# Optimization experiments

Measured on AMD Instinct MI355X. Metric: run time of the kernel, lower is better.

## Reference

```python
import jax, jax.numpy as jnp
import numpy as np

B, S, HID = 2, 2048, 1024
H, HKV, D = 16, 8, 128
G = H // HKV  # GQA group size
EPS = 1e-6
THETA = 1000000.0


def setup_inputs() -> dict:
    key = jax.random.key(0)
    ks = jax.random.split(key, 6)
    hidden_states = jax.random.normal(ks[0], (B, S, HID), dtype=jnp.float32)
    # causal boolean mask: True = attend
    attention_mask = jnp.tril(jnp.ones((S, S), dtype=bool))[None, None]
    # RoPE tables (HF convention: freqs duplicated across both halves)
    inv_freq = 1.0 / (THETA ** (jnp.arange(0, D, 2, dtype=jnp.float32) / D))
    ang = jnp.arange(S, dtype=jnp.float32)[:, None] * inv_freq[None, :]  # [S, D/2]
    emb = jnp.concatenate([ang, ang], axis=-1)  # [S, D]
    cos, sin = jnp.cos(emb), jnp.sin(emb)
    std = 0.02
    Wq = jax.random.normal(ks[1], (HID, H * D), dtype=jnp.float32) * std
    Wk = jax.random.normal(ks[2], (HID, HKV * D), dtype=jnp.float32) * std
    Wv = jax.random.normal(ks[3], (HID, HKV * D), dtype=jnp.float32) * std
    Wo = jax.random.normal(ks[4], (H * D, HID), dtype=jnp.float32) * std
    q_norm_w = jnp.ones((D,), dtype=jnp.float32)
    k_norm_w = jnp.ones((D,), dtype=jnp.float32)
    return {"hidden_states": hidden_states, "attention_mask": attention_mask,
            "cos": cos, "sin": sin, "Wq": Wq, "Wk": Wk, "Wv": Wv, "Wo": Wo,
            "q_norm_w": q_norm_w, "k_norm_w": k_norm_w}


def _rms_norm(x, w):
    var = jnp.mean(x * x, axis=-1, keepdims=True)
    return x * jax.lax.rsqrt(var + EPS) * w


def _rotate_half(x):
    x1, x2 = jnp.split(x, 2, axis=-1)
    return jnp.concatenate([-x2, x1], axis=-1)


def reference(hidden_states, attention_mask, cos, sin, Wq, Wk, Wv, Wo, q_norm_w, k_norm_w):
    b, s, _ = hidden_states.shape
    xq = (hidden_states @ Wq).reshape(b, s, H, D).transpose(0, 2, 1, 3)    # [B,H,S,D]
    xk = (hidden_states @ Wk).reshape(b, s, HKV, D).transpose(0, 2, 1, 3)  # [B,Hkv,S,D]
    xv = (hidden_states @ Wv).reshape(b, s, HKV, D).transpose(0, 2, 1, 3)  # [B,Hkv,S,D]
    xq = _rms_norm(xq, q_norm_w)
    xk = _rms_norm(xk, k_norm_w)
    c = cos[None, None]  # [1,1,S,D]
    si = sin[None, None]
    xq = xq * c + _rotate_half(xq) * si
    xk = xk * c + _rotate_half(xk) * si
    # GQA without materializing repeated KV: group q heads per kv head
    xqg = xq.reshape(b, HKV, G, s, D)
    scale = 1.0 / jnp.sqrt(jnp.asarray(D, dtype=xq.dtype))
    scores = jnp.einsum('bkgsd,bktd->bkgst', xqg, xk) * scale  # [B,Hkv,G,S,S]
    mask = attention_mask[:, :, None]  # [1,1,1,S,S]
    scores = jnp.where(mask, scores, jnp.asarray(-jnp.inf, dtype=scores.dtype))
    probs = jax.nn.softmax(scores, axis=-1)
    out = jnp.einsum('bkgst,bktd->bkgsd', probs, xv)  # [B,Hkv,G,S,D]
    out = out.reshape(b, H, s, D).transpose(0, 2, 1, 3).reshape(b, s, H * D)
    return out @ Wo
```

## Files before the change

### kernel.cpp

```cpp
#include <hip/hip_runtime.h>
#include <stdint.h>

#define B_ 2
#define S_ 2048
#define H_ 16
#define HKV_ 8
#define D_ 128
#define EPS_ 1e-6f
#define SCALE_ 0.08838834764831845f
#define QSZ_ 8388608
#define KSZ_ 4194304

typedef __attribute__((ext_vector_type(8))) __bf16 bf16x8;
typedef __attribute__((ext_vector_type(4))) float f32x4;
typedef __attribute__((ext_vector_type(16))) float f32x16;

static __device__ __forceinline__ uint16_t f2b(float f) {
  uint32_t u = __builtin_bit_cast(uint32_t, f);
  u += 0x7fffu + ((u >> 16) & 1u);
  return (uint16_t)(u >> 16);
}
static __device__ __forceinline__ float b2f(uint16_t b) {
  uint32_t u = ((uint32_t)b) << 16;
  return __builtin_bit_cast(float, u);
}

typedef const __attribute__((address_space(1))) uint32_t* gas_p;
typedef __attribute__((address_space(3))) uint32_t* las_p;
static __device__ __forceinline__ void gload16(const void* g, void* l) {
  __builtin_amdgcn_global_load_lds((gas_p)g, (las_p)l, 16, 0, 0);
}

__global__ void castk(const float* __restrict__ in, uint16_t* __restrict__ out) {
  int i = blockIdx.x * 256 + threadIdx.x;
  float4 f = ((const float4*)in)[i];
  uint2 o;
  o.x = (uint32_t)f2b(f.x) | ((uint32_t)f2b(f.y) << 16);
  o.y = (uint32_t)f2b(f.z) | ((uint32_t)f2b(f.w) << 16);
  ((uint2*)out)[i] = o;
}

__global__ void transcast(const float* __restrict__ Wm, uint16_t* __restrict__ Wt,
                          int K, int N) {
  __shared__ float t[32][33];
  int nb = blockIdx.x * 32, kb = blockIdx.y * 32;
  int tx = threadIdx.x & 31, ty = threadIdx.x >> 5;
  #pragma unroll
  for (int i = ty; i < 32; i += 8) t[i][tx] = Wm[(size_t)(kb + i) * N + nb + tx];
  __syncthreads();
  #pragma unroll
  for (int i = ty; i < 32; i += 8) Wt[(size_t)(nb + i) * K + kb + tx] = f2b(t[tx][i]);
}

__global__ __launch_bounds__(256) void vtrans(const uint16_t* __restrict__ Vin,
                                              uint16_t* __restrict__ Vt) {
  __shared__ uint16_t L[64 * 64];
  int s0 = blockIdx.x * 64, d0 = blockIdx.y * 64;
  const uint16_t* src = Vin + (size_t)blockIdx.z * S_ * D_;
  uint16_t* dst = Vt + (size_t)blockIdx.z * S_ * D_;
  int t = threadIdx.x;
  int rr = t >> 3, cb = t & 7;
  #pragma unroll
  for (int half = 0; half < 2; ++half) {
    int row = rr + half * 32;
    uint4 v = *(const uint4*)(src + (size_t)(s0 + row) * D_ + d0 + cb * 8);
    *(uint4*)(L + row * 64 + ((cb ^ (row & 7)) * 8)) = v;
  }
  __syncthreads();
  int dr = t >> 2, sc = (t & 3) * 16;
  union { uint16_t s[16]; uint4 q[2]; } u;
  #pragma unroll
  for (int j = 0; j < 16; ++j) {
    int s = sc + j;
    u.s[j] = L[s * 64 + (((dr >> 3) ^ (s & 7)) * 8) + (dr & 7)];
  }
  uint4* op = (uint4*)(dst + (size_t)(d0 + dr) * S_ + s0 + sc);
  op[0] = u.q[0];
  op[1] = u.q[1];
}

__global__ __launch_bounds__(256) void gemm_bt(const uint16_t* __restrict__ A,
                                               const uint16_t* __restrict__ Bt,
                                               void* __restrict__ Cout,
                                               int M, int N, int K, int mode) {
  __shared__ uint16_t Al[128 * 64];
  __shared__ uint16_t Bl[128 * 64];
  int tid = threadIdx.x;
  int lane = tid & 63, lr = lane & 15, g = lane >> 4;
  int w = tid >> 6, wm = w >> 1, wn = w & 1;
  int wbase = w * 64;
  int m0 = blockIdx.y * 128, n0 = blockIdx.x * 128;
  f32x4 acc[4][4] = {};
  for (int k0 = 0; k0 < K; k0 += 64) {
    __syncthreads();
    #pragma unroll
    for (int p = 0; p < 4; ++p) {
      int c = tid + p * 256;
      int row = c >> 3, cb = c & 7;
      int sc = (cb ^ (row & 7)) * 8;
      gload16(A + (size_t)(m0 + row) * K + k0 + sc, Al + (size_t)(p * 256 + wbase) * 8);
      gload16(Bt + (size_t)(n0 + row) * K + k0 + sc, Bl + (size_t)(p * 256 + wbase) * 8);
    }
    __syncthreads();
    #pragma unroll
    for (int ks = 0; ks < 2; ++ks) {
      bf16x8 af[4], bfr[4];
      #pragma unroll
      for (int mi = 0; mi < 4; ++mi) {
        int row = wm * 64 + mi * 16 + lr;
        af[mi] = *(bf16x8*)((char*)Al + row * 128 + ((ks * 64 + g * 16) ^ ((row & 7) << 4)));
      }
      #pragma unroll
      for (int ni = 0; ni < 4; ++ni) {
        int row = wn * 64 + ni * 16 + lr;
        bfr[ni] = *(bf16x8*)((char*)Bl + row * 128 + ((ks * 64 + g * 16) ^ ((row & 7) << 4)));
      }
      __builtin_amdgcn_s_setprio(1);
      #pragma unroll
      for (int mi = 0; mi < 4; ++mi)
        #pragma unroll
        for (int ni = 0; ni < 4; ++ni)
          acc[mi][ni] = __builtin_amdgcn_mfma_f32_16x16x32_bf16(af[mi], bfr[ni], acc[mi][ni], 0, 0, 0);
      __builtin_amdgcn_s_setprio(0);
    }
  }
  #pragma unroll
  for (int mi = 0; mi < 4; ++mi)
    #pragma unroll
    for (int ni = 0; ni < 4; ++ni)
      #pragma unroll
      for (int e = 0; e < 4; ++e) {
        int row = m0 + wm * 64 + mi * 16 + 4 * g + e;
        int col = n0 + wn * 64 + ni * 16 + lr;
        float v = acc[mi][ni][e];
        if (mode == 2) {
          ((float*)Cout)[(size_t)row * N + col] = v;
        } else {
          int bb = row >> 11, s = row & 2047;
          size_t off;
          if (col < 2048)
            off = (((size_t)(bb * 16 + (col >> 7))) * 2048 + s) * 128 + (col & 127);
          else if (col < 3072)
            off = QSZ_ + (((size_t)(bb * 8 + ((col - 2048) >> 7))) * 2048 + s) * 128 + (col & 127);
          else
            off = QSZ_ + KSZ_ + (((size_t)(bb * 8 + ((col - 3072) >> 7))) * 2048 + s) * 128 + (col & 127);
          ((uint16_t*)Cout)[off] = f2b(v);
        }
      }
}

__global__ void norm_rope(uint16_t* __restrict__ Qb, uint16_t* __restrict__ Kb,
                          const float* __restrict__ qw, const float* __restrict__ kw,
                          const float* __restrict__ cosr, const float* __restrict__ sinr) {
  int row = blockIdx.x * 4 + (threadIdx.x >> 6);
  int lane = threadIdx.x & 63;
  int hh = row % 24;
  int bs = row / 24;
  int b = bs >> 11, s = bs & 2047;
  uint16_t* ptr;
  const float* wv;
  float sc;
  if (hh < H_) { ptr = Qb + (((size_t)(b * H_ + hh)) * S_ + s) * D_; wv = qw; sc = SCALE_; }
  else         { ptr = Kb + (((size_t)(b * HKV_ + (hh - H_))) * S_ + s) * D_; wv = kw; sc = 1.0f; }
  float x1 = b2f(ptr[lane]), x2 = b2f(ptr[lane + 64]);
  float ss = x1 * x1 + x2 * x2;
  #pragma unroll
  for (int msk = 1; msk < 64; msk <<= 1) ss += __shfl_xor(ss, msk, 64);
  float r = rsqrtf(ss * (1.0f / 128.0f) + EPS_);
  float n1 = x1 * r * wv[lane], n2 = x2 * r * wv[lane + 64];
  float c1 = cosr[s * 128 + lane], s1 = sinr[s * 128 + lane];
  float c2 = cosr[s * 128 + lane + 64], s2 = sinr[s * 128 + lane + 64];
  ptr[lane]      = f2b((n1 * c1 - n2 * s1) * sc);
  ptr[lane + 64] = f2b((n2 * c2 + n1 * s2) * sc);
}

#define STAGE(BUF, KB) {                                                       \
  int kb64 = (KB) * 64;                                                        \
  _Pragma("unroll") for (int p2 = 0; p2 < 4; ++p2) {                           \
    int ck = p2 * 4 + w;                                                       \
    int krow = ck * 4 + (lane >> 4);                                           \
    int kg = (lane & 15) ^ (krow & 7);                                         \
    gload16(Kg + (size_t)(kb64 + krow) * D_ + kg * 8, Kl[BUF] + ck * 512);     \
    int vrow = ck * 8 + (lane >> 3);                                           \
    int vg = (lane & 7) ^ (vrow & 7);                                          \
    gload16(Vg + (size_t)vrow * S_ + kb64 + vg * 8, Vl[BUF] + ck * 512);       \
  } }

__global__ __launch_bounds__(256, 2) void attn_kernel(const uint16_t* __restrict__ Qb,
                                                      const uint16_t* __restrict__ Kb,
                                                      const uint16_t* __restrict__ Vtg,
                                                      uint16_t* __restrict__ out) {
  __shared__ uint16_t Kl[2][64 * 128];
  __shared__ uint16_t Vl[2][128 * 64];
  int tid = threadIdx.x, lane = tid & 63, w = tid >> 6;
  int ql = lane & 31, hi = lane >> 5;
  int bi = blockIdx.x;
  int qg = 15 - (bi >> 5);
  int rem = bi & 31;
  int bkv = rem >> 1, hsel = rem & 1;
  int b = bkv >> 3, kv = bkv & 7, h = kv * 2 + hsel;
  int qt = qg * 4 + w;
  int q0 = qt * 32;
  int mykb = qt >> 1;
  int kbmax = 2 * qg + 1;
  const uint16_t* Qg = Qb + ((size_t)(b * H_ + h)) * S_ * D_;
  const uint16_t* Kg = Kb + ((size_t)(b * HKV_ + kv)) * S_ * D_;
  const uint16_t* Vg = Vtg + ((size_t)(b * HKV_ + kv)) * S_ * D_;
  bf16x8 qf[8];
  #pragma unroll
  for (int t = 0; t < 8; ++t)
    qf[t] = *(const bf16x8*)(Qg + (size_t)(q0 + ql) * D_ + t * 16 + 8 * hi);
  f32x16 O[4] = {};
  float mrun = -__builtin_inff();
  float lrun = 0.f;
  STAGE(0, 0)
  for (int kb = 0; kb <= kbmax; ++kb) {
    int cur = kb & 1;
    __syncthreads();
    if (kb < kbmax) STAGE(cur ^ 1, kb + 1)
    if (kb <= mykb) {
      const uint16_t* KlC = Kl[cur];
      const uint16_t* VlC = Vl[cur];
      bool diag = (kb == mykb);
      bool skip2 = diag && ((qt & 1) == 0);
      float p0[16], p1[16];
      {
        bf16x8 kf[8];
        #pragma unroll
        for (int t = 0; t < 8; ++t)
          kf[t] = *(const bf16x8*)(KlC + ql * 128 + (((2 * t + hi) ^ (ql & 7)) * 8));
        f32x16 acc = {};
        __builtin_amdgcn_s_setprio(1);
        #pragma unroll
        for (int t = 0; t < 8; ++t)
          acc = __builtin_amdgcn_mfma_f32_32x32x16_bf16(kf[t], qf[t], acc, 0, 0, 0);
        __builtin_amdgcn_s_setprio(0);
        #pragma unroll
        for (int r = 0; r < 16; ++r) p0[r] = acc[r];
      }
      if (!skip2) {
        bf16x8 kf[8];
        #pragma unroll
        for (int t = 0; t < 8; ++t)
          kf[t] = *(const bf16x8*)(KlC + (32 + ql) * 128 + (((2 * t + hi) ^ (ql & 7)) * 8));
        f32x16 acc = {};
        __builtin_amdgcn_s_setprio(1);
        #pragma unroll
        for (int t = 0; t < 8; ++t)
          acc = __builtin_amdgcn_mfma_f32_32x32x16_bf16(kf[t], qf[t], acc, 0, 0, 0);
        __builtin_amdgcn_s_setprio(0);
        #pragma unroll
        for (int r = 0; r < 16; ++r) p1[r] = acc[r];
      }
      if (diag && !(qt & 1)) {
        #pragma unroll
        for (int r = 0; r < 16; ++r) {
          int kk = kb * 64 + 8 * (r >> 2) + 4 * hi + (r & 3);
          if (kk > q0 + ql) p0[r] = -__builtin_inff();
        }
      }
      if (diag && (qt & 1)) {
        #pragma unroll
        for (int r = 0; r < 16; ++r) {
          int kk = kb * 64 + 32 + 8 * (r >> 2) + 4 * hi + (r & 3);
          if (kk > q0 + ql) p1[r] = -__builtin_inff();
        }
      }
      float m8[8];
      #pragma unroll
      for (int i = 0; i < 8; ++i) m8[i] = fmaxf(p0[i], p0[i + 8]);
      if (!skip2) {
        #pragma unroll
        for (int i = 0; i < 8; ++i) m8[i] = fmaxf(m8[i], fmaxf(p1[i], p1[i + 8]));
      }
      float m4a = fmaxf(m8[0], m8[4]), m4b = fmaxf(m8[1], m8[5]);
      float m4c = fmaxf(m8[2], m8[6]), m4d = fmaxf(m8[3], m8[7]);
      float pmax = fmaxf(fmaxf(m4a, m4b), fmaxf(m4c, m4d));
      pmax = fmaxf(pmax, __shfl_xor(pmax, 32, 64));
      if (__any(pmax > mrun + 8.f)) {
        float mnew = fmaxf(mrun, pmax);
        float rs = __expf(mrun - mnew);
        lrun *= rs;
        #pragma unroll
        for (int r = 0; r < 16; ++r) {
          float rr = __shfl(rs, (r & 3) + 8 * (r >> 2) + 4 * hi, 64);
          #pragma unroll
          for (int dt = 0; dt < 4; ++dt) O[dt][r] *= rr;
        }
        mrun = mnew;
      }
      float ls = 0.f;
      union PW { uint32_t w[4]; bf16x8 v; } pa0, pa1;
      #pragma unroll
      for (int r = 0; r < 16; ++r) { p0[r] = __expf(p0[r] - mrun); ls += p0[r]; }
      {
        uint32_t uu[4][2];
        #pragma unroll
        for (int T = 0; T < 4; ++T) {
          asm("v_cvt_pk_bf16_f32 %0, %1, %2" : "=v"(uu[T][0]) : "v"(p0[4 * T]), "v"(p0[4 * T + 1]));
          asm("v_cvt_pk_bf16_f32 %0, %1, %2" : "=v"(uu[T][1]) : "v"(p0[4 * T + 2]), "v"(p0[4 * T + 3]));
        }
        uint32_t a = uu[0][0], bb2 = uu[1][0];
        asm("v_permlane32_swap_b32 %0, %1" : "+v"(a), "+v"(bb2));
        uint32_t c = uu[0][1], d = uu[1][1];
        asm("v_permlane32_swap_b32 %0, %1" : "+v"(c), "+v"(d));
        pa0.w[0] = a; pa0.w[1] = c; pa0.w[2] = bb2; pa0.w[3] = d;
        uint32_t a2 = uu[2][0], b2 = uu[3][0];
        asm("v_permlane32_swap_b32 %0, %1" : "+v"(a2), "+v"(b2));
        uint32_t c2 = uu[2][1], d2 = uu[3][1];
        asm("v_permlane32_swap_b32 %0, %1" : "+v"(c2), "+v"(d2));
        pa1.w[0] = a2; pa1.w[1] = c2; pa1.w[2] = b2; pa1.w[3] = d2;
      }
      __builtin_amdgcn_s_setprio(1);
      #pragma unroll
      for (int dt = 0; dt < 4; ++dt) {
        bf16x8 v0 = *(const bf16x8*)(VlC + (dt * 32 + ql) * 64 + (((0 + hi) ^ (ql & 7)) * 8));
        bf16x8 v1 = *(const bf16x8*)(VlC + (dt * 32 + ql) * 64 + (((2 + hi) ^ (ql & 7)) * 8));
        O[dt] = __builtin_amdgcn_mfma_f32_32x32x16_bf16(pa0.v, v0, O[dt], 0, 0, 0);
        O[dt] = __builtin_amdgcn_mfma_f32_32x32x16_bf16(pa1.v, v1, O[dt], 0, 0, 0);
      }
      __builtin_amdgcn_s_setprio(0);
      if (!skip2) {
        union PW pa2, pa3;
        #pragma unroll
        for (int r = 0; r < 16; ++r) { p1[r] = __expf(p1[r] - mrun); ls += p1[r]; }
        {
          uint32_t uu[4][2];
          #pragma unroll
          for (int T = 0; T < 4; ++T) {
            asm("v_cvt_pk_bf16_f32 %0, %1, %2" : "=v"(uu[T][0]) : "v"(p1[4 * T]), "v"(p1[4 * T + 1]));
            asm("v_cvt_pk_bf16_f32 %0, %1, %2" : "=v"(uu[T][1]) : "v"(p1[4 * T + 2]), "v"(p1[4 * T + 3]));
          }
          uint32_t a = uu[0][0], bb2 = uu[1][0];
          asm("v_permlane32_swap_b32 %0, %1" : "+v"(a), "+v"(bb2));
          uint32_t c = uu[0][1], d = uu[1][1];
          asm("v_permlane32_swap_b32 %0, %1" : "+v"(c), "+v"(d));
          pa2.w[0] = a; pa2.w[1] = c; pa2.w[2] = bb2; pa2.w[3] = d;
          uint32_t a2 = uu[2][0], b2 = uu[3][0];
          asm("v_permlane32_swap_b32 %0, %1" : "+v"(a2), "+v"(b2));
          uint32_t c2 = uu[2][1], d2 = uu[3][1];
          asm("v_permlane32_swap_b32 %0, %1" : "+v"(c2), "+v"(d2));
          pa3.w[0] = a2; pa3.w[1] = c2; pa3.w[2] = b2; pa3.w[3] = d2;
        }
        __builtin_amdgcn_s_setprio(1);
        #pragma unroll
        for (int dt = 0; dt < 4; ++dt) {
          bf16x8 v2 = *(const bf16x8*)(VlC + (dt * 32 + ql) * 64 + (((4 + hi) ^ (ql & 7)) * 8));
          bf16x8 v3 = *(const bf16x8*)(VlC + (dt * 32 + ql) * 64 + (((6 + hi) ^ (ql & 7)) * 8));
          O[dt] = __builtin_amdgcn_mfma_f32_32x32x16_bf16(pa2.v, v2, O[dt], 0, 0, 0);
          O[dt] = __builtin_amdgcn_mfma_f32_32x32x16_bf16(pa3.v, v3, O[dt], 0, 0, 0);
        }
        __builtin_amdgcn_s_setprio(0);
      }
      ls += __shfl_xor(ls, 32, 64);
      lrun += ls;
    }
  }
  float linv = 1.0f / lrun;
  #pragma unroll
  for (int r = 0; r < 16; ++r) {
    int qrl = (r & 3) + 8 * (r >> 2) + 4 * hi;
    float lr_ = __shfl(linv, qrl, 64);
    #pragma unroll
    for (int dt = 0; dt < 4; ++dt) {
      size_t o = ((size_t)(b * S_ + q0 + qrl)) * 2048 + h * 128 + dt * 32 + ql;
      out[o] = f2b(O[dt][r] * lr_);
    }
  }
}

extern "C" void kernel_launch(void* const* d_in, const int* in_sizes, int n_in,
                              void* d_out, int out_size, void* d_ws, size_t ws_size,
                              hipStream_t stream) {
  const float* hidden = (const float*)d_in[0];
  const float* cosr = (const float*)d_in[2];
  const float* sinr = (const float*)d_in[3];
  const float* Wq = (const float*)d_in[4];
  const float* Wk = (const float*)d_in[5];
  const float* Wv = (const float*)d_in[6];
  const float* Wo = (const float*)d_in[7];
  const float* qw = (const float*)d_in[8];
  const float* kw = (const float*)d_in[9];

  uint16_t* p = (uint16_t*)d_ws;
  uint16_t* Xb   = p; p += (size_t)4096 * 1024;
  uint16_t* Wqt  = p; p += (size_t)2048 * 1024;
  uint16_t* Wkt  = p; p += (size_t)1024 * 1024;
  uint16_t* Wvt  = p; p += (size_t)1024 * 1024;
  uint16_t* Wot  = p; p += (size_t)1024 * 2048;
  uint16_t* Qbuf = p; p += (size_t)B_ * H_ * S_ * D_;
  uint16_t* Kbuf = p; p += (size_t)B_ * HKV_ * S_ * D_;
  uint16_t* Vbuf = p; p += (size_t)B_ * HKV_ * S_ * D_;
  uint16_t* attn = p; p += (size_t)4096 * 2048;
  uint16_t* Vtb  = Xb;

  castk<<<4096, 256, 0, stream>>>(hidden, Xb);
  transcast<<<dim3(64, 32), 256, 0, stream>>>(Wq, Wqt, 1024, 2048);
  transcast<<<dim3(32, 32), 256, 0, stream>>>(Wk, Wkt, 1024, 1024);
  transcast<<<dim3(32, 32), 256, 0, stream>>>(Wv, Wvt, 1024, 1024);
  transcast<<<dim3(32, 64), 256, 0, stream>>>(Wo, Wot, 2048, 1024);
  gemm_bt<<<dim3(32, 32), 256, 0, stream>>>(Xb, Wqt, Qbuf, 4096, 4096, 1024, 3);
  vtrans<<<dim3(32, 2, 16), 256, 0, stream>>>(Vbuf, Vtb);
  norm_rope<<<24576, 256, 0, stream>>>(Qbuf, Kbuf, qw, kw, cosr, sinr);
  attn_kernel<<<512, 256, 0, stream>>>(Qbuf, Kbuf, Vtb, attn);
  gemm_bt<<<dim3(8, 32), 256, 0, stream>>>(attn, Wot, d_out, 4096, 1024, 2048, 2);
}
```

Before: 204.6 us.

## Add smaller-tile output GEMM and interleave causal attention block order

Adds a dedicated output-projection GEMM with 128x64 tiles, which launches 512 blocks instead of 256 so more of the GPU's compute units stay busy for the final fp32 projection. The attention grid mapping now sends the first 256 blocks to the heaviest query groups first and the second 256 to the lightest first. This is meant to balance causal work across the two waves of blocks. Smaller tiles reduce reuse per block and add redundant A loads.

```diff
diff --git a/kernel.cpp b/kernel.cpp
--- a/kernel.cpp
+++ b/kernel.cpp
@@ -149,6 +149,69 @@
       }
 }
 
+__global__ __launch_bounds__(256) void gemm_o(const uint16_t* __restrict__ A,
+                                              const uint16_t* __restrict__ Bt,
+                                              float* __restrict__ Cout,
+                                              int M, int N, int K) {
+  __shared__ uint16_t Al[128 * 64];
+  __shared__ uint16_t Bl[64 * 64];
+  int tid = threadIdx.x;
+  int lane = tid & 63, lr = lane & 15, g = lane >> 4;
+  int w = tid >> 6, wm = w >> 1, wn = w & 1;
+  int wbase = w * 64;
+  int m0 = blockIdx.y * 128, n0 = blockIdx.x * 64;
+  f32x4 acc[4][2] = {};
+  for (int k0 = 0; k0 < K; k0 += 64) {
+    __syncthreads();
+    #pragma unroll
+    for (int p = 0; p < 4; ++p) {
+      int c = tid + p * 256;
+      int row = c >> 3, cb = c & 7;
+      int sc = (cb ^ (row & 7)) * 8;
+      gload16(A + (size_t)(m0 + row) * K + k0 + sc, Al + (size_t)(p * 256 + wbase) * 8);
+    }
+    #pragma unroll
+    for (int p = 0; p < 2; ++p) {
+      int c = tid + p * 256;
+      int row = c >> 3, cb = c & 7;
+      int sc = (cb ^ (row & 7)) * 8;
+      gload16(Bt + (size_t)(n0 + row) * K + k0 + sc, Bl + (size_t)(p * 256 + wbase) * 8);
+    }
+    __syncthreads();
+    #pragma unroll
+    for (int ks = 0; ks < 2; ++ks) {
+      bf16x8 af[4], bfr[2];
+      #pragma unroll
+      for (int mi = 0; mi < 4; ++mi) {
+        int row = wm * 64 + mi * 16 + lr;
+        af[mi] = *(bf16x8*)((char*)Al + row * 128 + ((ks * 64 + g * 16) ^ ((row & 7) << 4)));
+      }
+      #pragma unroll
+      for (int ni = 0; ni < 2; ++ni) {
+        int row = wn * 32 + ni * 16 + lr;
+        bfr[ni] = *(bf16x8*)((char*)Bl + row * 128 + ((ks * 64 + g * 16) ^ ((row & 7) << 4)));
+      }
+      __builtin_amdgcn_s_setprio(1);
+      #pragma unroll
+      for (int mi = 0; mi < 4; ++mi)
+        #pragma unroll
+        for (int ni = 0; ni < 2; ++ni)
+          acc[mi][ni] = __builtin_amdgcn_mfma_f32_16x16x32_bf16(af[mi], bfr[ni], acc[mi][ni], 0, 0, 0);
+      __builtin_amdgcn_s_setprio(0);
+    }
+  }
+  #pragma unroll
+  for (int mi = 0; mi < 4; ++mi)
+    #pragma unroll
+    for (int ni = 0; ni < 2; ++ni)
+      #pragma unroll
+      for (int e = 0; e < 4; ++e) {
+        int row = m0 + wm * 64 + mi * 16 + 4 * g + e;
+        int col = n0 + wn * 32 + ni * 16 + lr;
+        Cout[(size_t)row * N + col] = acc[mi][ni][e];
+      }
+}
+
 __global__ void norm_rope(uint16_t* __restrict__ Qb, uint16_t* __restrict__ Kb,
                           const float* __restrict__ qw, const float* __restrict__ kw,
                           const float* __restrict__ cosr, const float* __restrict__ sinr) {
@@ -195,8 +258,11 @@
   int tid = threadIdx.x, lane = tid & 63, w = tid >> 6;
   int ql = lane & 31, hi = lane >> 5;
   int bi = blockIdx.x;
-  int qg = 15 - (bi >> 5);
-  int rem = bi & 31;
+  int biH = bi >> 8;
+  int j = bi & 255;
+  int qgl = j >> 5;
+  int qg = biH ? qgl : 15 - qgl;
+  int rem = j & 31;
   int bkv = rem >> 1, hsel = rem & 1;
   int b = bkv >> 3, kv = bkv & 7, h = kv * 2 + hsel;
   int qt = qg * 4 + w;
@@ -403,5 +469,5 @@
   vtrans<<<dim3(32, 2, 16), 256, 0, stream>>>(Vbuf, Vtb);
   norm_rope<<<24576, 256, 0, stream>>>(Qbuf, Kbuf, qw, kw, cosr, sinr);
   attn_kernel<<<512, 256, 0, stream>>>(Qbuf, Kbuf, Vtb, attn);
-  gemm_bt<<<dim3(8, 32), 256, 0, stream>>>(attn, Wot, d_out, 4096, 1024, 2048, 2);
-}
+  gemm_o<<<dim3(16, 32), 256, 0, stream>>>(attn, Wot, (float*)d_out, 4096, 1024, 2048);
+}
```

Measured after the change: 194.5 us. 4.9% less time.
